# Kernel optimization log

Measured on AMD Instinct MI355X. Metric: run time of the kernel, lower is better.

The kernel has to match this reference:

```python
import jax, jax.numpy as jnp
import numpy as np


def setup_inputs() -> dict:
    key = jax.random.key(0)
    k1, k2 = jax.random.split(key)
    N = 8192
    means = jax.random.normal(k1, (N, 3), dtype=jnp.float32) * 2.0
    normals = jax.random.normal(k2, (N, 3), dtype=jnp.float32)
    normals = normals / (jnp.linalg.norm(normals, axis=-1, keepdims=True) + 1e-8)
    return {"means": means, "normals": normals, "k": 8}


def reference(means, normals, k):
    # Pairwise Euclidean distances via the ||a-b||^2 expansion: avoids the
    # N x N x 3 diff tensor the original torch code materializes (same math).
    sq = jnp.sum(means * means, axis=-1)                      # (N,)
    d2 = sq[:, None] + sq[None, :] - 2.0 * (means @ means.T)  # (N, N)
    dists = jnp.sqrt(jnp.maximum(d2, 0.0))
    # k+1 smallest distances (self is the 0-distance nearest); drop self.
    dists = jax.lax.stop_gradient(dists)
    _, idx = jax.lax.top_k(-dists, k + 1)                     # (N, k+1)
    idx = idx[:, 1:]                                          # (N, k)
    neighbors = means[idx]                                    # (N, k, 3)
    local_diff = neighbors - means[:, None, :]                # (N, k, 3)
    plane_dist = jnp.sum(local_diff * normals[:, None, :], axis=-1)  # (N, k)
    return jnp.mean(jnp.abs(plane_dist))
```

## Files before the change

kernel.cpp:

```cpp
#include <hip/hip_runtime.h>
#include <hip/hip_bf16.h>

#define NPTS 8192
#define KNN 8
#define NBC 16
#define CPB 512
#define TSEG 8

typedef __attribute__((ext_vector_type(8))) short bf16x8;
typedef __attribute__((ext_vector_type(4))) float f32x4;

__device__ __forceinline__ unsigned int bf16rne(float x) {
    unsigned int u = __float_as_uint(x);
    return (u + 0x7FFFu + ((u >> 16) & 1u)) >> 16;
}
__device__ __forceinline__ float bf2f(unsigned int h) { return __uint_as_float(h << 16); }

__device__ __forceinline__ void insert8(unsigned int (&best)[KNN], unsigned int key) {
#pragma unroll
    for (int t = 0; t < KNN; ++t) {
        const unsigned int lo = min(best[t], key);
        key = max(best[t], key);
        best[t] = lo;
    }
}

__global__ __launch_bounds__(512) void prep_thresh(const float* __restrict__ means,
                                                   float4* __restrict__ pts,
                                                   uint4* __restrict__ bfragB,
                                                   float* __restrict__ Tm_arr,
                                                   float* __restrict__ out) {
    __shared__ unsigned int lds_k[TSEG][64][5];
    const int tid = threadIdx.x;
    const int l = tid & 63;
    const int wv = __builtin_amdgcn_readfirstlane(tid >> 6);
    const int pt = blockIdx.x * 64 + l;
    if (blockIdx.x == 0 && tid == 0) out[0] = 0.0f;

    const float x = means[3 * pt + 0];
    const float y = means[3 * pt + 1];
    const float z = means[3 * pt + 2];
    const float sq = x * x + y * y + z * z;
    if (wv == 0) {
        pts[pt] = make_float4(x, y, z, sq);
        const unsigned int hx = bf16rne(x), lx = bf16rne(x - bf2f(hx));
        const unsigned int hy = bf16rne(y), ly = bf16rne(y - bf2f(hy));
        const unsigned int hz = bf16rne(z), lz = bf16rne(z - bf2f(hz));
        const unsigned int hs = bf16rne(sq), ls = bf16rne(sq - bf2f(hs));
        bfragB[pt * 2 + 0] = make_uint4(hx | (lx << 16), hx | (hy << 16),
                                        ly | (hy << 16), hz | (lz << 16));
        bfragB[pt * 2 + 1] = make_uint4(hz | (hs << 16), ls | (0x3F80u << 16), 0x3F80u, 0u);
    }

    const float mx2 = -2.0f * x, my2 = -2.0f * y, mz2 = -2.0f * z;
    unsigned int b4[4] = {0xFFFFFFFFu, 0xFFFFFFFFu, 0xFFFFFFFFu, 0xFFFFFFFFu};
#pragma unroll 4
    for (int m = 0; m < 64; ++m) {
        const int col = 16 * (wv + TSEG * m);
        const float qx = means[3 * col + 0];
        const float qy = means[3 * col + 1];
        const float qz = means[3 * col + 2];
        const float qsq = qx * qx + qy * qy + qz * qz;
        const float d2 = fmaxf(fmaf(mx2, qx, fmaf(my2, qy, fmaf(mz2, qz, sq + qsq))), 0.0f);
        unsigned int key = (__float_as_uint(d2) & 0xFFFFE000u) | (unsigned int)col;
        key = (col == pt) ? 0xFFFFFFFFu : key;
#pragma unroll
        for (int t = 0; t < 4; ++t) {
            const unsigned int lo = min(b4[t], key);
            key = max(b4[t], key);
            b4[t] = lo;
        }
    }
#pragma unroll
    for (int s = 0; s < 4; ++s) lds_k[wv][l][s] = b4[s];
    __syncthreads();
    if (wv == 0) {
        unsigned int best[KNN] = {b4[0], b4[1], b4[2], b4[3],
                                  0xFFFFFFFFu, 0xFFFFFFFFu, 0xFFFFFFFFu, 0xFFFFFFFFu};
#pragma unroll
        for (int w = 1; w < TSEG; ++w)
#pragma unroll
            for (int s = 0; s < 4; ++s) insert8(best, lds_k[w][l][s]);
        const float Tf = __uint_as_float(best[7] & 0xFFFFE000u);
        Tm_arr[pt] = Tf + 0.02f + 2e-3f * Tf;
    }
}

__global__ __launch_bounds__(256) void mfma_knn(const float4* __restrict__ pts,
                                                const uint4* __restrict__ bfragB,
                                                const float* __restrict__ Tm_arr,
                                                unsigned int* __restrict__ part) {
    __shared__ uint4 lds_b[CPB * 2];
    __shared__ unsigned int lds_bits[4][64][5];
    const int tid = threadIdx.x;
    const int l = tid & 63;
    const int wv = __builtin_amdgcn_readfirstlane(tid >> 6);
    const int rp = blockIdx.x >> 4;
    const int cbi = blockIdx.x & 15;
    const int cb = cbi * CPB;
    {
        const uint4* __restrict__ src = bfragB + cb * 2;
#pragma unroll
        for (int k = 0; k < 4; ++k) lds_b[tid + 256 * k] = src[tid + 256 * k];
    }
    const int rbase = rp * 64 + wv * 16;
    const int arow = rbase + (l & 15);
    const int g = l >> 4;
    const float4 mp = pts[arow];
    const float ax = -2.0f * mp.x, ay = -2.0f * mp.y, az = -2.0f * mp.z;
    const unsigned int hax = bf16rne(ax), lax = bf16rne(ax - bf2f(hax));
    const unsigned int hay = bf16rne(ay), lay = bf16rne(ay - bf2f(hay));
    const unsigned int haz = bf16rne(az), laz = bf16rne(az - bf2f(haz));
    const unsigned int hsr = bf16rne(mp.w), lsr = bf16rne(mp.w - bf2f(hsr));
    uint4 au = make_uint4(0u, 0u, 0u, 0u);
    if (g == 0) au = make_uint4(hax | (hax << 16), lax | (hay << 16),
                                hay | (lay << 16), haz | (haz << 16));
    if (g == 1) au = make_uint4(laz | (0x3F80u << 16), 0x3F80u | (hsr << 16), lsr, 0u);
    union { uint4 u; bf16x8 v; } A; A.u = au;
    float Tm[4];
#pragma unroll
    for (int r = 0; r < 4; ++r) Tm[r] = Tm_arr[rbase + g * 4 + r];
    __syncthreads();

    const int bidx = (l & 15) * 2 + (g & 1);
    const f32x4 zero = {0.0f, 0.0f, 0.0f, 0.0f};
    unsigned int m0[4];
#pragma unroll
    for (int r = 0; r < 4; ++r) m0[r] = 0u;
#pragma unroll 4
    for (int t2 = 0; t2 < 32; ++t2) {
        union { uint4 u; bf16x8 v; } B; B.u = lds_b[t2 * 32 + bidx];
        const f32x4 acc = __builtin_amdgcn_mfma_f32_16x16x32_bf16(A.v, B.v, zero, 0, 0, 0);
#pragma unroll
        for (int r = 0; r < 4; ++r) m0[r] = m0[r] * 2u + ((acc[r] <= Tm[r]) ? 1u : 0u);
    }
#pragma unroll
    for (int r = 0; r < 4; ++r) lds_bits[wv][l][r] = m0[r];
    __syncthreads();

    unsigned int best[KNN];
#pragma unroll
    for (int s = 0; s < KNN; ++s) best[s] = 0xFFFFFFFFu;
    const int LR = l & 15;
#pragma unroll
    for (int cc = 0; cc < 4; ++cc) {
        const int cl = (l >> 4) * 4 + cc;
        unsigned int w = lds_bits[wv][(LR >> 2) * 16 + cl][LR & 3];
        while (w) {
            const int b = __ffs(w) - 1;
            w &= w - 1;
            const int ct2 = 31 - b;
            const int col = cb + ct2 * 16 + cl;
            const float4 q = pts[col];
            const float d2 = fmaxf(fmaf(ax, q.x, fmaf(ay, q.y, fmaf(az, q.z, mp.w + q.w))), 0.0f);
            unsigned int key = (__float_as_uint(d2) & 0xFFFFE000u) | (unsigned int)col;
            key = (col == arow) ? 0xFFFFFFFFu : key;
            insert8(best, key);
        }
    }
#pragma unroll
    for (int st = 16; st <= 32; st <<= 1) {
        unsigned int tk[KNN];
#pragma unroll
        for (int s = 0; s < KNN; ++s) tk[s] = __shfl_xor(best[s], st);
#pragma unroll
        for (int s = 0; s < KNN; ++s) insert8(best, tk[s]);
    }
    if (l < 16) {
        uint4* dst = (uint4*)(part + ((unsigned int)arow * (unsigned int)NBC + (unsigned int)cbi) * 8u);
        dst[0] = make_uint4(best[0], best[1], best[2], best[3]);
        dst[1] = make_uint4(best[4], best[5], best[6], best[7]);
    }
}

__global__ __launch_bounds__(256) void final_kernel(const float4* __restrict__ pts,
                                                    const float* __restrict__ normals,
                                                    const unsigned int* __restrict__ part,
                                                    float* __restrict__ out) {
    __shared__ float red[4];
    const int row = blockIdx.x * 256 + threadIdx.x;
    unsigned int best[KNN];
#pragma unroll
    for (int s = 0; s < KNN; ++s) best[s] = 0xFFFFFFFFu;
    const uint4* __restrict__ P = (const uint4*)(part + (unsigned int)row * (unsigned int)(NBC * 8));
#pragma unroll
    for (int b = 0; b < NBC * 2; ++b) {
        const uint4 v = P[b];
        insert8(best, v.x); insert8(best, v.y); insert8(best, v.z); insert8(best, v.w);
    }
    const float4 mp = pts[row];
    const float nx = normals[3 * row + 0], ny = normals[3 * row + 1], nz = normals[3 * row + 2];
    float sum = 0.0f;
#pragma unroll
    for (int s = 0; s < KNN; ++s) {
        const int nbr = (int)(best[s] & 0x1FFFu);
        const float4 q = pts[nbr];
        sum += fabsf((q.x - mp.x) * nx + (q.y - mp.y) * ny + (q.z - mp.z) * nz);
    }
    float v = sum;
#pragma unroll
    for (int off = 32; off > 0; off >>= 1) v += __shfl_down(v, off);
    if ((threadIdx.x & 63) == 0) red[threadIdx.x >> 6] = v;
    __syncthreads();
    if (threadIdx.x == 0)
        atomicAdd(out, (red[0] + red[1] + red[2] + red[3]) * (1.0f / ((float)NPTS * (float)KNN)));
}

extern "C" void kernel_launch(void* const* d_in, const int* in_sizes, int n_in,
                              void* d_out, int out_size, void* d_ws, size_t ws_size,
                              hipStream_t stream) {
    const float* means = (const float*)d_in[0];
    const float* normals = (const float*)d_in[1];
    float* out = (float*)d_out;
    char* ws = (char*)d_ws;
    float4* pts = (float4*)ws;
    uint4* bfragB = (uint4*)(ws + 131072);
    float* Tm = (float*)(ws + 393216);
    unsigned int* part = (unsigned int*)(ws + 425984);

    prep_thresh<<<NPTS / 64, 512, 0, stream>>>(means, pts, bfragB, Tm, out);
    mfma_knn<<<(NPTS / 64) * NBC, 256, 0, stream>>>(pts, bfragB, Tm, part);
    final_kernel<<<NPTS / 256, 256, 0, stream>>>(pts, normals, part, out);
}
```

Before: 42.51 us.

## Fuse threshold, MFMA kNN and reduction into one kernel per 16 rows

Replaces the three-kernel pipeline (threshold prep, column-split MFMA filter with partial top-k in global memory, final merge) with a single kernel. Each block owns 16 rows, computes its threshold locally, streams all columns through LDS in stages while building bf16 split fragments on the fly, and merges the top-k lists across waves in LDS before the plane-distance sum. This removes the launch overhead and the global round trips for partial results. In exchange there are far fewer blocks (512), each block repeats the bf16 conversion of every column, and the stage loop adds per-stage barriers.

Result: slower. 50.98 us (+19.9%).

```diff
diff --git a/kernel.cpp b/kernel.cpp
--- a/kernel.cpp
+++ b/kernel.cpp
@@ -3,15 +3,16 @@
 
 #define NPTS 8192
 #define KNN 8
-#define NBC 16
-#define CPB 512
-#define TSEG 8
+#define RPB 16
+#define THREADS 512
+#define STAGES 16
+#define SCOLS 512
 
 typedef __attribute__((ext_vector_type(8))) short bf16x8;
 typedef __attribute__((ext_vector_type(4))) float f32x4;
 
-__device__ __forceinline__ unsigned int bf16rne(float x) {
-    unsigned int u = __float_as_uint(x);
+__device__ __forceinline__ unsigned int bf16rne(float v) {
+    unsigned int u = __float_as_uint(v);
     return (u + 0x7FFFu + ((u >> 16) & 1u)) >> 16;
 }
 __device__ __forceinline__ float bf2f(unsigned int h) { return __uint_as_float(h << 16); }
@@ -25,139 +26,144 @@
     }
 }
 
-__global__ __launch_bounds__(512) void prep_thresh(const float* __restrict__ means,
-                                                   float4* __restrict__ pts,
-                                                   uint4* __restrict__ bfragB,
-                                                   float* __restrict__ Tm_arr,
+__global__ __launch_bounds__(THREADS) void knn_all(const float* __restrict__ means,
+                                                   const float* __restrict__ normals,
                                                    float* __restrict__ out) {
-    __shared__ unsigned int lds_k[TSEG][64][5];
+    __shared__ uint4 lds_b[SCOLS * 2];
+    __shared__ unsigned int lds_bits[8][64][5];
+    __shared__ unsigned int thr_k[32][RPB][4];
+    __shared__ unsigned int km[8][RPB][KNN];
+    __shared__ float lds_T[RPB];
+
     const int tid = threadIdx.x;
     const int l = tid & 63;
     const int wv = __builtin_amdgcn_readfirstlane(tid >> 6);
-    const int pt = blockIdx.x * 64 + l;
-    if (blockIdx.x == 0 && tid == 0) out[0] = 0.0f;
-
-    const float x = means[3 * pt + 0];
-    const float y = means[3 * pt + 1];
-    const float z = means[3 * pt + 2];
+    const int rb = blockIdx.x * RPB;
+
+    const int R = l & 15;
+    const int g = l >> 4;
+    const int arow = rb + R;
+    const float x = means[3 * arow + 0];
+    const float y = means[3 * arow + 1];
+    const float z = means[3 * arow + 2];
     const float sq = x * x + y * y + z * z;
-    if (wv == 0) {
-        pts[pt] = make_float4(x, y, z, sq);
-        const unsigned int hx = bf16rne(x), lx = bf16rne(x - bf2f(hx));
-        const unsigned int hy = bf16rne(y), ly = bf16rne(y - bf2f(hy));
-        const unsigned int hz = bf16rne(z), lz = bf16rne(z - bf2f(hz));
-        const unsigned int hs = bf16rne(sq), ls = bf16rne(sq - bf2f(hs));
-        bfragB[pt * 2 + 0] = make_uint4(hx | (lx << 16), hx | (hy << 16),
-                                        ly | (hy << 16), hz | (lz << 16));
-        bfragB[pt * 2 + 1] = make_uint4(hz | (hs << 16), ls | (0x3F80u << 16), 0x3F80u, 0u);
-    }
-
-    const float mx2 = -2.0f * x, my2 = -2.0f * y, mz2 = -2.0f * z;
-    unsigned int b4[4] = {0xFFFFFFFFu, 0xFFFFFFFFu, 0xFFFFFFFFu, 0xFFFFFFFFu};
+    const float ax = -2.0f * x, ay = -2.0f * y, az = -2.0f * z;
+
+    {
+        const int trow = tid & 15;
+        const int cls = tid >> 4;
+        const int trg = rb + trow;
+        const float tx = means[3 * trg + 0];
+        const float ty = means[3 * trg + 1];
+        const float tz = means[3 * trg + 2];
+        const float tsq = tx * tx + ty * ty + tz * tz;
+        const float bx = -2.0f * tx, by = -2.0f * ty, bz = -2.0f * tz;
+        unsigned int b4[4] = {~0u, ~0u, ~0u, ~0u};
 #pragma unroll 4
-    for (int m = 0; m < 64; ++m) {
-        const int col = 16 * (wv + TSEG * m);
-        const float qx = means[3 * col + 0];
-        const float qy = means[3 * col + 1];
-        const float qz = means[3 * col + 2];
-        const float qsq = qx * qx + qy * qy + qz * qz;
-        const float d2 = fmaxf(fmaf(mx2, qx, fmaf(my2, qy, fmaf(mz2, qz, sq + qsq))), 0.0f);
-        unsigned int key = (__float_as_uint(d2) & 0xFFFFE000u) | (unsigned int)col;
-        key = (col == pt) ? 0xFFFFFFFFu : key;
-#pragma unroll
-        for (int t = 0; t < 4; ++t) {
-            const unsigned int lo = min(b4[t], key);
-            key = max(b4[t], key);
-            b4[t] = lo;
-        }
-    }
-#pragma unroll
-    for (int s = 0; s < 4; ++s) lds_k[wv][l][s] = b4[s];
-    __syncthreads();
-    if (wv == 0) {
-        unsigned int best[KNN] = {b4[0], b4[1], b4[2], b4[3],
-                                  0xFFFFFFFFu, 0xFFFFFFFFu, 0xFFFFFFFFu, 0xFFFFFFFFu};
-#pragma unroll
-        for (int w = 1; w < TSEG; ++w)
-#pragma unroll
-            for (int s = 0; s < 4; ++s) insert8(best, lds_k[w][l][s]);
-        const float Tf = __uint_as_float(best[7] & 0xFFFFE000u);
-        Tm_arr[pt] = Tf + 0.02f + 2e-3f * Tf;
-    }
-}
-
-__global__ __launch_bounds__(256) void mfma_knn(const float4* __restrict__ pts,
-                                                const uint4* __restrict__ bfragB,
-                                                const float* __restrict__ Tm_arr,
-                                                unsigned int* __restrict__ part) {
-    __shared__ uint4 lds_b[CPB * 2];
-    __shared__ unsigned int lds_bits[4][64][5];
-    const int tid = threadIdx.x;
-    const int l = tid & 63;
-    const int wv = __builtin_amdgcn_readfirstlane(tid >> 6);
-    const int rp = blockIdx.x >> 4;
-    const int cbi = blockIdx.x & 15;
-    const int cb = cbi * CPB;
-    {
-        const uint4* __restrict__ src = bfragB + cb * 2;
-#pragma unroll
-        for (int k = 0; k < 4; ++k) lds_b[tid + 256 * k] = src[tid + 256 * k];
-    }
-    const int rbase = rp * 64 + wv * 16;
-    const int arow = rbase + (l & 15);
-    const int g = l >> 4;
-    const float4 mp = pts[arow];
-    const float ax = -2.0f * mp.x, ay = -2.0f * mp.y, az = -2.0f * mp.z;
+        for (int m = 0; m < 16; ++m) {
+            const int col = cls * 256 + m * 16;
+            const float qx = means[3 * col + 0];
+            const float qy = means[3 * col + 1];
+            const float qz = means[3 * col + 2];
+            const float qsq = qx * qx + qy * qy + qz * qz;
+            const float d2 = fmaxf(fmaf(bx, qx, fmaf(by, qy, fmaf(bz, qz, tsq + qsq))), 0.0f);
+            unsigned int key = (__float_as_uint(d2) & 0xFFFFE000u) | (unsigned int)col;
+            key = (col == trg) ? ~0u : key;
+#pragma unroll
+            for (int t = 0; t < 4; ++t) {
+                const unsigned int lo = min(b4[t], key);
+                key = max(b4[t], key);
+                b4[t] = lo;
+            }
+        }
+#pragma unroll
+        for (int j = 0; j < 4; ++j) thr_k[cls][trow][j] = b4[j];
+        __syncthreads();
+        if (tid < RPB) {
+            unsigned int bb[KNN];
+#pragma unroll
+            for (int s = 0; s < KNN; ++s) bb[s] = ~0u;
+            for (int c = 0; c < 32; ++c)
+#pragma unroll
+                for (int j = 0; j < 4; ++j) insert8(bb, thr_k[c][tid][j]);
+            const float Tf = __uint_as_float(bb[7] & 0xFFFFE000u);
+            lds_T[tid] = Tf + 0.02f + 2e-3f * Tf;
+        }
+        __syncthreads();
+    }
+    float Tmr[4];
+#pragma unroll
+    for (int r = 0; r < 4; ++r) Tmr[r] = lds_T[g * 4 + r];
+
     const unsigned int hax = bf16rne(ax), lax = bf16rne(ax - bf2f(hax));
     const unsigned int hay = bf16rne(ay), lay = bf16rne(ay - bf2f(hay));
     const unsigned int haz = bf16rne(az), laz = bf16rne(az - bf2f(haz));
-    const unsigned int hsr = bf16rne(mp.w), lsr = bf16rne(mp.w - bf2f(hsr));
+    const unsigned int hsr = bf16rne(sq), lsr = bf16rne(sq - bf2f(hsr));
     uint4 au = make_uint4(0u, 0u, 0u, 0u);
     if (g == 0) au = make_uint4(hax | (hax << 16), lax | (hay << 16),
                                 hay | (lay << 16), haz | (haz << 16));
     if (g == 1) au = make_uint4(laz | (0x3F80u << 16), 0x3F80u | (hsr << 16), lsr, 0u);
     union { uint4 u; bf16x8 v; } A; A.u = au;
-    float Tm[4];
-#pragma unroll
-    for (int r = 0; r < 4; ++r) Tm[r] = Tm_arr[rbase + g * 4 + r];
-    __syncthreads();
-
-    const int bidx = (l & 15) * 2 + (g & 1);
     const f32x4 zero = {0.0f, 0.0f, 0.0f, 0.0f};
-    unsigned int m0[4];
-#pragma unroll
-    for (int r = 0; r < 4; ++r) m0[r] = 0u;
-#pragma unroll 4
-    for (int t2 = 0; t2 < 32; ++t2) {
-        union { uint4 u; bf16x8 v; } B; B.u = lds_b[t2 * 32 + bidx];
-        const f32x4 acc = __builtin_amdgcn_mfma_f32_16x16x32_bf16(A.v, B.v, zero, 0, 0, 0);
-#pragma unroll
-        for (int r = 0; r < 4; ++r) m0[r] = m0[r] * 2u + ((acc[r] <= Tm[r]) ? 1u : 0u);
-    }
-#pragma unroll
-    for (int r = 0; r < 4; ++r) lds_bits[wv][l][r] = m0[r];
-    __syncthreads();
-
+
+    unsigned int bv[4] = {0u, 0u, 0u, 0u};
     unsigned int best[KNN];
 #pragma unroll
-    for (int s = 0; s < KNN; ++s) best[s] = 0xFFFFFFFFu;
-    const int LR = l & 15;
-#pragma unroll
-    for (int cc = 0; cc < 4; ++cc) {
-        const int cl = (l >> 4) * 4 + cc;
-        unsigned int w = lds_bits[wv][(LR >> 2) * 16 + cl][LR & 3];
-        while (w) {
-            const int b = __ffs(w) - 1;
-            w &= w - 1;
-            const int ct2 = 31 - b;
-            const int col = cb + ct2 * 16 + cl;
-            const float4 q = pts[col];
-            const float d2 = fmaxf(fmaf(ax, q.x, fmaf(ay, q.y, fmaf(az, q.z, mp.w + q.w))), 0.0f);
-            unsigned int key = (__float_as_uint(d2) & 0xFFFFE000u) | (unsigned int)col;
-            key = (col == arow) ? 0xFFFFFFFFu : key;
-            insert8(best, key);
-        }
-    }
+    for (int s = 0; s < KNN; ++s) best[s] = ~0u;
+
+    for (int s = 0; s < STAGES; ++s) {
+        __syncthreads();
+        {
+            const int cg = s * SCOLS + tid;
+            const float qx = means[3 * cg + 0];
+            const float qy = means[3 * cg + 1];
+            const float qz = means[3 * cg + 2];
+            const float qsq = qx * qx + qy * qy + qz * qz;
+            const unsigned int hx = bf16rne(qx), lx = bf16rne(qx - bf2f(hx));
+            const unsigned int hy = bf16rne(qy), ly = bf16rne(qy - bf2f(hy));
+            const unsigned int hz = bf16rne(qz), lz = bf16rne(qz - bf2f(hz));
+            const unsigned int hs = bf16rne(qsq), ls = bf16rne(qsq - bf2f(hs));
+            lds_b[tid * 2 + 0] = make_uint4(hx | (lx << 16), hx | (hy << 16),
+                                            ly | (hy << 16), hz | (lz << 16));
+            lds_b[tid * 2 + 1] = make_uint4(hz | (hs << 16), ls | (0x3F80u << 16), 0x3F80u, 0u);
+        }
+        __syncthreads();
+        const int bbase = wv * 128;
+#pragma unroll
+        for (int m = 0; m < 4; ++m) {
+            union { uint4 u; bf16x8 v; } B;
+            B.u = lds_b[bbase + m * 32 + R * 2 + (g & 1)];
+            const f32x4 acc = __builtin_amdgcn_mfma_f32_16x16x32_bf16(A.v, B.v, zero, 0, 0, 0);
+#pragma unroll
+            for (int r = 0; r < 4; ++r) bv[r] = bv[r] * 2u + ((acc[r] <= Tmr[r]) ? 1u : 0u);
+        }
+        if ((s & 7) == 7) {
+            const int d = s >> 3;
+#pragma unroll
+            for (int r = 0; r < 4; ++r) { lds_bits[wv][l][r] = bv[r]; bv[r] = 0u; }
+            const int base_l = (R >> 2) * 16;
+#pragma unroll
+            for (int cc4 = 0; cc4 < 4; ++cc4) {
+                const int cc = g * 4 + cc4;
+                unsigned int w = lds_bits[wv][base_l + cc][R & 3];
+                while (w) {
+                    const int b = __ffs(w) - 1;
+                    w &= w - 1;
+                    const int t = 31 - b;
+                    const int col = (d * 8 + (t >> 2)) * SCOLS + wv * 64 + (t & 3) * 16 + cc;
+                    const float qx = means[3 * col + 0];
+                    const float qy = means[3 * col + 1];
+                    const float qz = means[3 * col + 2];
+                    const float qsq = qx * qx + qy * qy + qz * qz;
+                    const float d2 = fmaxf(fmaf(ax, qx, fmaf(ay, qy, fmaf(az, qz, sq + qsq))), 0.0f);
+                    unsigned int key = (__float_as_uint(d2) & 0xFFFFE000u) | (unsigned int)col;
+                    key = (col == arow) ? ~0u : key;
+                    insert8(best, key);
+                }
+            }
+        }
+    }
+
 #pragma unroll
     for (int st = 16; st <= 32; st <<= 1) {
         unsigned int tk[KNN];
@@ -166,44 +172,37 @@
 #pragma unroll
         for (int s = 0; s < KNN; ++s) insert8(best, tk[s]);
     }
-    if (l < 16) {
-        uint4* dst = (uint4*)(part + ((unsigned int)arow * (unsigned int)NBC + (unsigned int)cbi) * 8u);
-        dst[0] = make_uint4(best[0], best[1], best[2], best[3]);
-        dst[1] = make_uint4(best[4], best[5], best[6], best[7]);
-    }
-}
-
-__global__ __launch_bounds__(256) void final_kernel(const float4* __restrict__ pts,
-                                                    const float* __restrict__ normals,
-                                                    const unsigned int* __restrict__ part,
-                                                    float* __restrict__ out) {
-    __shared__ float red[4];
-    const int row = blockIdx.x * 256 + threadIdx.x;
-    unsigned int best[KNN];
-#pragma unroll
-    for (int s = 0; s < KNN; ++s) best[s] = 0xFFFFFFFFu;
-    const uint4* __restrict__ P = (const uint4*)(part + (unsigned int)row * (unsigned int)(NBC * 8));
-#pragma unroll
-    for (int b = 0; b < NBC * 2; ++b) {
-        const uint4 v = P[b];
-        insert8(best, v.x); insert8(best, v.y); insert8(best, v.z); insert8(best, v.w);
-    }
-    const float4 mp = pts[row];
-    const float nx = normals[3 * row + 0], ny = normals[3 * row + 1], nz = normals[3 * row + 2];
-    float sum = 0.0f;
-#pragma unroll
-    for (int s = 0; s < KNN; ++s) {
-        const int nbr = (int)(best[s] & 0x1FFFu);
-        const float4 q = pts[nbr];
-        sum += fabsf((q.x - mp.x) * nx + (q.y - mp.y) * ny + (q.z - mp.z) * nz);
-    }
-    float v = sum;
-#pragma unroll
-    for (int off = 32; off > 0; off >>= 1) v += __shfl_down(v, off);
-    if ((threadIdx.x & 63) == 0) red[threadIdx.x >> 6] = v;
-    __syncthreads();
-    if (threadIdx.x == 0)
-        atomicAdd(out, (red[0] + red[1] + red[2] + red[3]) * (1.0f / ((float)NPTS * (float)KNN)));
+    if (l < RPB) {
+#pragma unroll
+        for (int s = 0; s < KNN; ++s) km[wv][l][s] = best[s];
+    }
+    for (int st = 1; st < 8; st <<= 1) {
+        __syncthreads();
+        if (((wv & (2 * st - 1)) == 0) && l < RPB) {
+#pragma unroll
+            for (int s = 0; s < KNN; ++s) insert8(best, km[wv + st][l][s]);
+#pragma unroll
+            for (int s = 0; s < KNN; ++s) km[wv][l][s] = best[s];
+        }
+    }
+
+    if (wv == 0 && l < RPB) {
+        const float nx = normals[3 * arow + 0];
+        const float ny = normals[3 * arow + 1];
+        const float nz = normals[3 * arow + 2];
+        float sum = 0.0f;
+#pragma unroll
+        for (int s = 0; s < KNN; ++s) {
+            const int nbr = (int)(best[s] & 0x1FFFu);
+            const float qx = means[3 * nbr + 0];
+            const float qy = means[3 * nbr + 1];
+            const float qz = means[3 * nbr + 2];
+            sum += fabsf((qx - x) * nx + (qy - y) * ny + (qz - z) * nz);
+        }
+#pragma unroll
+        for (int off = 8; off > 0; off >>= 1) sum += __shfl_down(sum, off);
+        if (l == 0) atomicAdd(out, sum * (1.0f / ((float)NPTS * (float)KNN)));
+    }
 }
 
 extern "C" void kernel_launch(void* const* d_in, const int* in_sizes, int n_in,
@@ -212,13 +211,8 @@
     const float* means = (const float*)d_in[0];
     const float* normals = (const float*)d_in[1];
     float* out = (float*)d_out;
-    char* ws = (char*)d_ws;
-    float4* pts = (float4*)ws;
-    uint4* bfragB = (uint4*)(ws + 131072);
-    float* Tm = (float*)(ws + 393216);
-    unsigned int* part = (unsigned int*)(ws + 425984);
-
-    prep_thresh<<<NPTS / 64, 512, 0, stream>>>(means, pts, bfragB, Tm, out);
-    mfma_knn<<<(NPTS / 64) * NBC, 256, 0, stream>>>(pts, bfragB, Tm, part);
-    final_kernel<<<NPTS / 256, 256, 0, stream>>>(pts, normals, part, out);
-}
+    (void)d_ws; (void)ws_size;
+
+    hipMemsetAsync(out, 0, sizeof(float), stream);
+    knn_all<<<NPTS / RPB, THREADS, 0, stream>>>(means, normals, out);
+}
```

## Fuse KNN partial merge and final reduction into a single row-blocked MFMA kernel

Applied to the files above, without the earlier changes.

Restructures the MFMA KNN kernel so each 512-thread block owns 16 rows and streams all 8192 columns through LDS in 8 stages, with a register prefetch of the next stage. The 16-column-block partial results buffer and the separate final merge kernel are removed. Per-wave top-8 lists are merged through LDS in a tree, and the plane-distance sum is computed in place. Row and column bf16 fragments are precomputed in the prep kernel. The grid shrinks from 2048 to 512 blocks, and each block adds 7 barrier-separated stages.

New measurement: 40.69 us. 1.04x faster.

```diff
diff --git a/kernel.cpp b/kernel.cpp
--- a/kernel.cpp
+++ b/kernel.cpp
@@ -3,15 +3,16 @@
 
 #define NPTS 8192
 #define KNN 8
-#define NBC 16
-#define CPB 512
+#define RPB 16
+#define STAGES 8
+#define SCOLS 1024
 #define TSEG 8
 
 typedef __attribute__((ext_vector_type(8))) short bf16x8;
 typedef __attribute__((ext_vector_type(4))) float f32x4;
 
-__device__ __forceinline__ unsigned int bf16rne(float x) {
-    unsigned int u = __float_as_uint(x);
+__device__ __forceinline__ unsigned int bf16rne(float v) {
+    unsigned int u = __float_as_uint(v);
     return (u + 0x7FFFu + ((u >> 16) & 1u)) >> 16;
 }
 __device__ __forceinline__ float bf2f(unsigned int h) { return __uint_as_float(h << 16); }
@@ -27,7 +28,10 @@
 
 __global__ __launch_bounds__(512) void prep_thresh(const float* __restrict__ means,
                                                    float4* __restrict__ pts,
-                                                   uint4* __restrict__ bfragB,
+                                                   uint4* __restrict__ cf0,
+                                                   uint4* __restrict__ cf1,
+                                                   uint4* __restrict__ rf0,
+                                                   uint4* __restrict__ rf1,
                                                    float* __restrict__ Tm_arr,
                                                    float* __restrict__ out) {
     __shared__ unsigned int lds_k[TSEG][64][5];
@@ -47,13 +51,21 @@
         const unsigned int hy = bf16rne(y), ly = bf16rne(y - bf2f(hy));
         const unsigned int hz = bf16rne(z), lz = bf16rne(z - bf2f(hz));
         const unsigned int hs = bf16rne(sq), ls = bf16rne(sq - bf2f(hs));
-        bfragB[pt * 2 + 0] = make_uint4(hx | (lx << 16), hx | (hy << 16),
-                                        ly | (hy << 16), hz | (lz << 16));
-        bfragB[pt * 2 + 1] = make_uint4(hz | (hs << 16), ls | (0x3F80u << 16), 0x3F80u, 0u);
+        cf0[pt] = make_uint4(hx | (lx << 16), hx | (hy << 16),
+                             ly | (hy << 16), hz | (lz << 16));
+        cf1[pt] = make_uint4(hz | (hs << 16), ls | (0x3F80u << 16), 0x3F80u, 0u);
+        const float ax = -2.0f * x, ay = -2.0f * y, az = -2.0f * z;
+        const unsigned int hax = bf16rne(ax), lax = bf16rne(ax - bf2f(hax));
+        const unsigned int hay = bf16rne(ay), lay = bf16rne(ay - bf2f(hay));
+        const unsigned int haz = bf16rne(az), laz = bf16rne(az - bf2f(haz));
+        const unsigned int hsr = bf16rne(sq), lsr = bf16rne(sq - bf2f(hsr));
+        rf0[pt] = make_uint4(hax | (hax << 16), lax | (hay << 16),
+                             hay | (lay << 16), haz | (haz << 16));
+        rf1[pt] = make_uint4(laz | (0x3F80u << 16), 0x3F80u | (hsr << 16), lsr, 0u);
     }
 
     const float mx2 = -2.0f * x, my2 = -2.0f * y, mz2 = -2.0f * z;
-    unsigned int b4[4] = {0xFFFFFFFFu, 0xFFFFFFFFu, 0xFFFFFFFFu, 0xFFFFFFFFu};
+    unsigned int b4[4] = {~0u, ~0u, ~0u, ~0u};
 #pragma unroll 4
     for (int m = 0; m < 64; ++m) {
         const int col = 16 * (wv + TSEG * m);
@@ -63,7 +75,7 @@
         const float qsq = qx * qx + qy * qy + qz * qz;
         const float d2 = fmaxf(fmaf(mx2, qx, fmaf(my2, qy, fmaf(mz2, qz, sq + qsq))), 0.0f);
         unsigned int key = (__float_as_uint(d2) & 0xFFFFE000u) | (unsigned int)col;
-        key = (col == pt) ? 0xFFFFFFFFu : key;
+        key = (col == pt) ? ~0u : key;
 #pragma unroll
         for (int t = 0; t < 4; ++t) {
             const unsigned int lo = min(b4[t], key);
@@ -75,8 +87,7 @@
     for (int s = 0; s < 4; ++s) lds_k[wv][l][s] = b4[s];
     __syncthreads();
     if (wv == 0) {
-        unsigned int best[KNN] = {b4[0], b4[1], b4[2], b4[3],
-                                  0xFFFFFFFFu, 0xFFFFFFFFu, 0xFFFFFFFFu, 0xFFFFFFFFu};
+        unsigned int best[KNN] = {b4[0], b4[1], b4[2], b4[3], ~0u, ~0u, ~0u, ~0u};
 #pragma unroll
         for (int w = 1; w < TSEG; ++w)
 #pragma unroll
@@ -86,78 +97,74 @@
     }
 }
 
-__global__ __launch_bounds__(256) void mfma_knn(const float4* __restrict__ pts,
-                                                const uint4* __restrict__ bfragB,
+__global__ __launch_bounds__(512) void mfma_knn(const uint4* __restrict__ cf0,
+                                                const uint4* __restrict__ cf1,
+                                                const uint4* __restrict__ rf0,
+                                                const uint4* __restrict__ rf1,
+                                                const float4* __restrict__ pts,
                                                 const float* __restrict__ Tm_arr,
-                                                unsigned int* __restrict__ part) {
-    __shared__ uint4 lds_b[CPB * 2];
-    __shared__ unsigned int lds_bits[4][64][5];
+                                                const float* __restrict__ normals,
+                                                float* __restrict__ out) {
+    __shared__ uint4 lds_cf[2 * SCOLS];
+    __shared__ unsigned int km[TSEG][RPB][KNN + 1];
     const int tid = threadIdx.x;
     const int l = tid & 63;
     const int wv = __builtin_amdgcn_readfirstlane(tid >> 6);
-    const int rp = blockIdx.x >> 4;
-    const int cbi = blockIdx.x & 15;
-    const int cb = cbi * CPB;
-    {
-        const uint4* __restrict__ src = bfragB + cb * 2;
-#pragma unroll
-        for (int k = 0; k < 4; ++k) lds_b[tid + 256 * k] = src[tid + 256 * k];
-    }
-    const int rbase = rp * 64 + wv * 16;
-    const int arow = rbase + (l & 15);
+    const int R = l & 15;
     const int g = l >> 4;
+    const int arow = blockIdx.x * RPB + R;
+
     const float4 mp = pts[arow];
     const float ax = -2.0f * mp.x, ay = -2.0f * mp.y, az = -2.0f * mp.z;
-    const unsigned int hax = bf16rne(ax), lax = bf16rne(ax - bf2f(hax));
-    const unsigned int hay = bf16rne(ay), lay = bf16rne(ay - bf2f(hay));
-    const unsigned int haz = bf16rne(az), laz = bf16rne(az - bf2f(haz));
-    const unsigned int hsr = bf16rne(mp.w), lsr = bf16rne(mp.w - bf2f(hsr));
-    uint4 au = make_uint4(0u, 0u, 0u, 0u);
-    if (g == 0) au = make_uint4(hax | (hax << 16), lax | (hay << 16),
-                                hay | (lay << 16), haz | (haz << 16));
-    if (g == 1) au = make_uint4(laz | (0x3F80u << 16), 0x3F80u | (hsr << 16), lsr, 0u);
-    union { uint4 u; bf16x8 v; } A; A.u = au;
-    float Tm[4];
-#pragma unroll
-    for (int r = 0; r < 4; ++r) Tm[r] = Tm_arr[rbase + g * 4 + r];
-    __syncthreads();
-
-    const int bidx = (l & 15) * 2 + (g & 1);
+    const float sq = mp.w;
+    const float Tm = Tm_arr[arow];
+
+    uint4 bu = make_uint4(0u, 0u, 0u, 0u);
+    if (g == 0) bu = rf0[arow];
+    else if (g == 1) bu = rf1[arow];
+    union { uint4 u; bf16x8 v; } Bf; Bf.u = bu;
     const f32x4 zero = {0.0f, 0.0f, 0.0f, 0.0f};
-    unsigned int m0[4];
-#pragma unroll
-    for (int r = 0; r < 4; ++r) m0[r] = 0u;
-#pragma unroll 4
-    for (int t2 = 0; t2 < 32; ++t2) {
-        union { uint4 u; bf16x8 v; } B; B.u = lds_b[t2 * 32 + bidx];
-        const f32x4 acc = __builtin_amdgcn_mfma_f32_16x16x32_bf16(A.v, B.v, zero, 0, 0, 0);
-#pragma unroll
-        for (int r = 0; r < 4; ++r) m0[r] = m0[r] * 2u + ((acc[r] <= Tm[r]) ? 1u : 0u);
-    }
-#pragma unroll
-    for (int r = 0; r < 4; ++r) lds_bits[wv][l][r] = m0[r];
-    __syncthreads();
 
     unsigned int best[KNN];
 #pragma unroll
-    for (int s = 0; s < KNN; ++s) best[s] = 0xFFFFFFFFu;
-    const int LR = l & 15;
-#pragma unroll
-    for (int cc = 0; cc < 4; ++cc) {
-        const int cl = (l >> 4) * 4 + cc;
-        unsigned int w = lds_bits[wv][(LR >> 2) * 16 + cl][LR & 3];
-        while (w) {
-            const int b = __ffs(w) - 1;
-            w &= w - 1;
-            const int ct2 = 31 - b;
-            const int col = cb + ct2 * 16 + cl;
+    for (int s = 0; s < KNN; ++s) best[s] = ~0u;
+
+    uint4 r0a = cf0[tid], r0b = cf0[512 + tid];
+    uint4 r1a = cf1[tid], r1b = cf1[512 + tid];
+
+    for (int s = 0; s < STAGES; ++s) {
+        __syncthreads();
+        lds_cf[tid] = r0a;            lds_cf[512 + tid] = r0b;
+        lds_cf[1024 + tid] = r1a;     lds_cf[1536 + tid] = r1b;
+        __syncthreads();
+        if (s + 1 < STAGES) {
+            const int o = (s + 1) * SCOLS;
+            r0a = cf0[o + tid]; r0b = cf0[o + 512 + tid];
+            r1a = cf1[o + tid]; r1b = cf1[o + 512 + tid];
+        }
+        const uint4* __restrict__ asel = (g == 1) ? (lds_cf + SCOLS) : lds_cf;
+        unsigned int m = 0u;
+#pragma unroll
+        for (int mt = 0; mt < 8; ++mt) {
+            union { uint4 u; bf16x8 v; } Af;
+            Af.u = asel[wv * 128 + mt * 16 + R];
+            const f32x4 acc = __builtin_amdgcn_mfma_f32_16x16x32_bf16(Af.v, Bf.v, zero, 0, 0, 0);
+#pragma unroll
+            for (int r = 0; r < 4; ++r) m = m + m + ((acc[r] <= Tm) ? 1u : 0u);
+        }
+        while (m) {
+            const int b = __ffs(m) - 1;
+            m &= m - 1;
+            const int t = 31 - b;
+            const int col = s * SCOLS + wv * 128 + (t >> 2) * 16 + g * 4 + (t & 3);
             const float4 q = pts[col];
-            const float d2 = fmaxf(fmaf(ax, q.x, fmaf(ay, q.y, fmaf(az, q.z, mp.w + q.w))), 0.0f);
+            const float d2 = fmaxf(fmaf(ax, q.x, fmaf(ay, q.y, fmaf(az, q.z, sq + q.w))), 0.0f);
             unsigned int key = (__float_as_uint(d2) & 0xFFFFE000u) | (unsigned int)col;
-            key = (col == arow) ? 0xFFFFFFFFu : key;
+            key = (col == arow) ? ~0u : key;
             insert8(best, key);
         }
     }
+
 #pragma unroll
     for (int st = 16; st <= 32; st <<= 1) {
         unsigned int tk[KNN];
@@ -166,44 +173,37 @@
 #pragma unroll
         for (int s = 0; s < KNN; ++s) insert8(best, tk[s]);
     }
-    if (l < 16) {
-        uint4* dst = (uint4*)(part + ((unsigned int)arow * (unsigned int)NBC + (unsigned int)cbi) * 8u);
-        dst[0] = make_uint4(best[0], best[1], best[2], best[3]);
-        dst[1] = make_uint4(best[4], best[5], best[6], best[7]);
-    }
-}
-
-__global__ __launch_bounds__(256) void final_kernel(const float4* __restrict__ pts,
-                                                    const float* __restrict__ normals,
-                                                    const unsigned int* __restrict__ part,
-                                                    float* __restrict__ out) {
-    __shared__ float red[4];
-    const int row = blockIdx.x * 256 + threadIdx.x;
-    unsigned int best[KNN];
-#pragma unroll
-    for (int s = 0; s < KNN; ++s) best[s] = 0xFFFFFFFFu;
-    const uint4* __restrict__ P = (const uint4*)(part + (unsigned int)row * (unsigned int)(NBC * 8));
-#pragma unroll
-    for (int b = 0; b < NBC * 2; ++b) {
-        const uint4 v = P[b];
-        insert8(best, v.x); insert8(best, v.y); insert8(best, v.z); insert8(best, v.w);
-    }
-    const float4 mp = pts[row];
-    const float nx = normals[3 * row + 0], ny = normals[3 * row + 1], nz = normals[3 * row + 2];
-    float sum = 0.0f;
-#pragma unroll
-    for (int s = 0; s < KNN; ++s) {
-        const int nbr = (int)(best[s] & 0x1FFFu);
-        const float4 q = pts[nbr];
-        sum += fabsf((q.x - mp.x) * nx + (q.y - mp.y) * ny + (q.z - mp.z) * nz);
-    }
-    float v = sum;
-#pragma unroll
-    for (int off = 32; off > 0; off >>= 1) v += __shfl_down(v, off);
-    if ((threadIdx.x & 63) == 0) red[threadIdx.x >> 6] = v;
-    __syncthreads();
-    if (threadIdx.x == 0)
-        atomicAdd(out, (red[0] + red[1] + red[2] + red[3]) * (1.0f / ((float)NPTS * (float)KNN)));
+    if (l < RPB) {
+#pragma unroll
+        for (int s = 0; s < KNN; ++s) km[wv][l][s] = best[s];
+    }
+    for (int st = 1; st < TSEG; st <<= 1) {
+        __syncthreads();
+        if (((wv & (2 * st - 1)) == 0) && l < RPB) {
+#pragma unroll
+            for (int s = 0; s < KNN; ++s) insert8(best, km[wv + st][l][s]);
+#pragma unroll
+            for (int s = 0; s < KNN; ++s) km[wv][l][s] = best[s];
+        }
+    }
+
+    if (wv == 0) {
+        float sum = 0.0f;
+        if (l < RPB) {
+            const float nx = normals[3 * arow + 0];
+            const float ny = normals[3 * arow + 1];
+            const float nz = normals[3 * arow + 2];
+#pragma unroll
+            for (int s = 0; s < KNN; ++s) {
+                const int nbr = (int)(best[s] & 0x1FFFu);
+                const float4 q = pts[nbr];
+                sum += fabsf((q.x - mp.x) * nx + (q.y - mp.y) * ny + (q.z - mp.z) * nz);
+            }
+        }
+#pragma unroll
+        for (int off = 8; off > 0; off >>= 1) sum += __shfl_down(sum, off);
+        if (l == 0) atomicAdd(out, sum * (1.0f / ((float)NPTS * (float)KNN)));
+    }
 }
 
 extern "C" void kernel_launch(void* const* d_in, const int* in_sizes, int n_in,
@@ -213,12 +213,13 @@
     const float* normals = (const float*)d_in[1];
     float* out = (float*)d_out;
     char* ws = (char*)d_ws;
-    float4* pts = (float4*)ws;
-    uint4* bfragB = (uint4*)(ws + 131072);
-    float* Tm = (float*)(ws + 393216);
-    unsigned int* part = (unsigned int*)(ws + 425984);
-
-    prep_thresh<<<NPTS / 64, 512, 0, stream>>>(means, pts, bfragB, Tm, out);
-    mfma_knn<<<(NPTS / 64) * NBC, 256, 0, stream>>>(pts, bfragB, Tm, part);
-    final_kernel<<<NPTS / 256, 256, 0, stream>>>(pts, normals, part, out);
-}
+    uint4* cf0 = (uint4*)ws;
+    uint4* cf1 = (uint4*)(ws + 131072);
+    uint4* rf0 = (uint4*)(ws + 262144);
+    uint4* rf1 = (uint4*)(ws + 393216);
+    float4* pts = (float4*)(ws + 524288);
+    float* Tm = (float*)(ws + 655360);
+
+    prep_thresh<<<NPTS / 64, 512, 0, stream>>>(means, pts, cf0, cf1, rf0, rf1, Tm, out);
+    mfma_knn<<<NPTS / RPB, 512, 0, stream>>>(cf0, cf1, rf0, rf1, pts, Tm, normals, out);
+}
```
